# Kernel tuning notes

Measured on AMD Instinct MI355X. Metric: run time of the kernel, lower is better.

## Reference

```python
import jax, jax.numpy as jnp
import numpy as np

N, E, D, H, C, B, G = 50000, 800000, 128, 256, 40, 3, 2
EPS = 1e-5


def setup_inputs() -> dict:
    key = jax.random.key(0)
    ks = jax.random.split(key, 32)
    rn = lambda k, s: jax.random.normal(k, s, dtype=jnp.float32)
    inp = {
        'x': rn(ks[0], (N, D)),
        'edge_index': jax.random.randint(ks[1], (2, E), 0, N, dtype=jnp.int64),
        'Wp': rn(ks[2], (D, H)), 'bp': rn(ks[3], (H,)),
        'W1l': rn(ks[4], (B, H, H)), 'b1l': rn(ks[5], (B, H)), 'W1r': rn(ks[6], (B, H, H)),
        'W2l': rn(ks[7], (B, H, H)), 'b2l': rn(ks[8], (B, H)), 'W2r': rn(ks[9], (B, H, H)),
        'bn1_g': rn(ks[10], (B, H)), 'bn1_b': rn(ks[11], (B, H)), 'bn1_m': rn(ks[12], (B, H)),
        'bn1_v': jax.random.uniform(ks[13], (B, H), dtype=jnp.float32),
        'bn2_g': rn(ks[14], (B, H)), 'bn2_b': rn(ks[15], (B, H)), 'bn2_m': rn(ks[16], (B, H)),
        'bn2_v': jax.random.uniform(ks[17], (B, H), dtype=jnp.float32),
        'gate_W': rn(ks[18], (G, H, H)), 'gate_b': rn(ks[19], (G, H)),
        'Wc1': rn(ks[20], (H, H // 2)), 'bc1': rn(ks[21], (H // 2,)),
        'Wc2': rn(ks[22], (H // 2, C)), 'bc2': rn(ks[23], (C,)),
    }
    return inp


def _sage(x, src, dst, Wl, bl, Wr):
    # PyG SAGEConv (mean aggr): lin_l(mean_{j in N(i)} x_j) + lin_r(x_i)
    agg = jax.ops.segment_sum(x[src], dst, num_segments=N)  # [N,H]
    cnt = jax.ops.segment_sum(jnp.ones((src.shape[0],), x.dtype), dst, num_segments=N)
    mean = agg / jnp.maximum(cnt, 1.0)[:, None]
    return mean @ Wl + bl + x @ Wr


def _bn(x, g, b, m, v):
    return (x - m) * (g * jax.lax.rsqrt(v + EPS)) + b


def reference(x, edge_index, Wp, bp, W1l, b1l, W1r, W2l, b2l, W2r,
              bn1_g, bn1_b, bn1_m, bn1_v, bn2_g, bn2_b, bn2_m, bn2_v,
              gate_W, gate_b, Wc1, bc1, Wc2, bc2):
    src, dst = edge_index[0], edge_index[1]
    prev = x @ Wp + bp  # input projection [N,H]
    for i in range(B):
        res = prev
        h = jax.nn.relu(_bn(_sage(prev, src, dst, W1l[i], b1l[i], W1r[i]),
                            bn1_g[i], bn1_b[i], bn1_m[i], bn1_v[i]))
        h = jax.nn.relu(_bn(_sage(h, src, dst, W2l[i], b2l[i], W2r[i]),
                            bn2_g[i], bn2_b[i], bn2_m[i], bn2_v[i]))
        cur = h + res
        if i > 0:
            gate = jax.nn.sigmoid(prev @ gate_W[i - 1] + gate_b[i - 1])
            cur = gate * prev + (1.0 - gate) * cur
        prev = cur
    return jax.nn.relu(prev @ Wc1 + bc1) @ Wc2 + bc2  # [N,C]
```

## Files before the change

kernel.cpp:

```cpp
#include <hip/hip_runtime.h>
#include <hip/hip_bf16.h>
#include <cstdint>

#define NNODES 50000
#define MPAD   50048
#define NEDGES 800000
#define DIN 128
#define HID 256
#define NCLS 40
#define NBLK 3
#define EPSV 1e-5f

typedef __bf16 bf16x8 __attribute__((ext_vector_type(8)));
typedef float  f32x4  __attribute__((ext_vector_type(4)));
typedef unsigned short us4v __attribute__((ext_vector_type(4)));
typedef unsigned short us8v __attribute__((ext_vector_type(8)));

__device__ __forceinline__ unsigned short bf_rtn(float x) {
  unsigned u = __float_as_uint(x);
  return (unsigned short)((u + 0x7fffu + ((u >> 16) & 1u)) >> 16);
}
__device__ __forceinline__ float bf_f(unsigned short h) {
  return __uint_as_float((unsigned)h << 16);
}
__device__ __forceinline__ void split4(float4 a, us4v& h, us4v& m, us4v& l) {
  float v[4] = {a.x, a.y, a.z, a.w};
#pragma unroll
  for (int i = 0; i < 4; i++) {
    unsigned short hh = bf_rtn(v[i]);
    float r1 = v[i] - bf_f(hh);
    unsigned short mm = bf_rtn(r1);
    float r2 = r1 - bf_f(mm);
    h[i] = hh; m[i] = mm; l[i] = bf_rtn(r2);
  }
}

__device__ __forceinline__ void glds16(const void* gsrc, void* ldst) {
  __builtin_amdgcn_global_load_lds((const __attribute__((address_space(1))) void*)gsrc,
                                   (__attribute__((address_space(3))) void*)ldst,
                                   16, 0, 0);
}

__global__ void hist_kernel(const int* __restrict__ dst, int* __restrict__ cnt, int E) {
  int e = blockIdx.x * blockDim.x + threadIdx.x;
  if (e < E) atomicAdd(&cnt[dst[e]], 1);
}

__global__ void scan_kernel(const int* __restrict__ cnt, int* __restrict__ row_ptr,
                            float* __restrict__ inv_cnt, int N) {
  __shared__ int sums[1024];
  int t = threadIdx.x;
  int chunk = (N + 1023) >> 10;
  int beg = t * chunk;
  int end = beg + chunk; if (end > N) end = N;
  int s = 0;
  for (int i = beg; i < end; ++i) s += cnt[i];
  sums[t] = s;
  __syncthreads();
  for (int off = 1; off < 1024; off <<= 1) {
    int v = 0;
    if (t >= off) v = sums[t - off];
    __syncthreads();
    sums[t] += v;
    __syncthreads();
  }
  int run = (t == 0) ? 0 : sums[t - 1];
  for (int i = beg; i < end; ++i) {
    row_ptr[i] = run;
    int c = cnt[i];
    inv_cnt[i] = 1.0f / (float)(c > 0 ? c : 1);
    run += c;
  }
  if (t == 1023) row_ptr[N] = run;
}

__global__ void fill_kernel(const int* __restrict__ src, const int* __restrict__ dst,
                            const int* __restrict__ row_ptr, int* __restrict__ fillc,
                            int* __restrict__ col, int E) {
  int e = blockIdx.x * blockDim.x + threadIdx.x;
  if (e < E) {
    int d = dst[e];
    int pos = atomicAdd(&fillc[d], 1);
    col[row_ptr[d] + pos] = src[e];
  }
}

__global__ __launch_bounds__(256)
void agg_kernel(const float* __restrict__ x, float* __restrict__ out,
                const int* __restrict__ row_ptr, const int* __restrict__ col,
                const float* __restrict__ inv_cnt) {
  int n = blockIdx.x;
  int h = threadIdx.x;
  int beg = row_ptr[n], end = row_ptr[n + 1];
  float s = 0.0f;
  for (int j = beg; j < end; ++j) {
    int c = col[j];
    s += x[(long)c * HID + h];
  }
  out[(long)n * HID + h] = s * inv_cnt[n];
}

__global__ void fold_kernel(const float* __restrict__ b1l, const float* __restrict__ g1,
                            const float* __restrict__ bb1, const float* __restrict__ m1,
                            const float* __restrict__ v1,
                            const float* __restrict__ b2l, const float* __restrict__ g2,
                            const float* __restrict__ bb2, const float* __restrict__ m2,
                            const float* __restrict__ v2,
                            float* __restrict__ S1, float* __restrict__ T1,
                            float* __restrict__ S2, float* __restrict__ T2) {
  int idx = blockIdx.x * 256 + threadIdx.x;
  float s1 = g1[idx] * rsqrtf(v1[idx] + EPSV);
  S1[idx] = s1;
  T1[idx] = (b1l[idx] - m1[idx]) * s1 + bb1[idx];
  float s2 = g2[idx] * rsqrtf(v2[idx] + EPSV);
  S2[idx] = s2;
  T2[idx] = (b2l[idx] - m2[idx]) * s2 + bb2[idx];
}

#define PREP_TOTAL 368640
struct PrepDescs {
  const float* src[16];
  unsigned dst_off[16];
  int N[16];
  int cum[16];
};
__global__ __launch_bounds__(256)
void prep_kernel(PrepDescs pd, char* out) {
  int i = blockIdx.x * 256 + threadIdx.x;
  if (i >= PREP_TOTAL) return;
  int j = 0;
  while (i >= pd.cum[j]) j++;
  int li = i - (j ? pd.cum[j - 1] : 0);
  int c = li % 12;
  int t = li / 12;
  int N = pd.N[j];
  int n = t % N;
  int kt = t / N;
  const float* src = pd.src[j];
  char* base = out + pd.dst_off[j] + (size_t)kt * N * 192;
  int p, k8;
  size_t addr;
  if (c < 8) {
    int d = c ^ (n & 7);
    p = d >> 2; k8 = d & 3;
    addr = (size_t)n * 128 + (size_t)c * 16;
  } else {
    p = 2; k8 = c - 8;
    addr = (size_t)N * 128 + ((size_t)k8 * N + n) * 16;
  }
  us8v v;
#pragma unroll
  for (int xj = 0; xj < 8; xj++) {
    float w = src[(size_t)(kt * 32 + k8 * 8 + xj) * N + n];
    unsigned short h = bf_rtn(w);
    if (p == 0) { v[xj] = h; continue; }
    float r1 = w - bf_f(h);
    unsigned short m = bf_rtn(r1);
    v[xj] = (p == 1) ? m : bf_rtn(r1 - bf_f(m));
  }
  *reinterpret_cast<us8v*>(base + addr) = v;
}

template<int BM, int BN, bool GATED>
__global__ __launch_bounds__(512)
void gemm_mfma(const float* __restrict__ A1, const char* __restrict__ B1, int K1,
               const float* __restrict__ A2, const char* __restrict__ B2, int K2,
               const char* __restrict__ BG, const float* __restrict__ Gb,
               const float* __restrict__ Sc, const float* __restrict__ Tc,
               const float* __restrict__ resid, float* __restrict__ C,
               int Mguard, int do_relu) {
  constexpr int WN = BN / 64;
  constexpr int WM = 8 / WN;
  constexpr int RB = BM / WM;
  constexpr int MT = RB / 16;
  constexpr int APITCH = 104;
  constexpr int AL = (BM * 32) / 2048;
  constexpr int NG = (BN * 24) / 1024;
  __shared__ __align__(16) unsigned short A_lds[2][BM][APITCH];
  __shared__ __align__(16) char B_lds[2][BN * 192];
  const int tid  = threadIdx.x;
  const int wv   = tid >> 6;
  const int lane = tid & 63;
  const int l15  = lane & 15;
  const int quad = lane >> 4;
  const int wm   = wv / WN;
  const int wn   = wv % WN;
  const int m0   = blockIdx.x * BM;
  const int sr   = tid >> 3;
  const int skc  = (tid & 7) * 4;

  f32x4 acc1[MT][4];
#pragma unroll
  for (int i = 0; i < MT; i++)
#pragma unroll
    for (int j = 0; j < 4; j++) acc1[i][j] = (f32x4){0.f, 0.f, 0.f, 0.f};
  f32x4 acc2[GATED ? MT : 1][GATED ? 4 : 1];
  if constexpr (GATED) {
#pragma unroll
    for (int i = 0; i < MT; i++)
#pragma unroll
      for (int j = 0; j < 4; j++) acc2[i][j] = (f32x4){0.f, 0.f, 0.f, 0.f};
  }

  int buf = 0;

  auto issueB = [&](const char* Bp, int kt, int b) {
    const char* bsrc = Bp + (size_t)kt * (BN * 192) + wv * (BN * 24) + (size_t)lane * 16;
    char* bdst = &B_lds[b][wv * (BN * 24)];
#pragma unroll
    for (int j = 0; j < NG; ++j)
      glds16(bsrc + j * 1024, bdst + j * 1024);
  };
  auto storeA = [&](float4 (&a)[AL], int b) {
#pragma unroll
    for (int i = 0; i < AL; i++) {
      us4v h4, m4, l4;
      split4(a[i], h4, m4, l4);
      unsigned short* rp = &A_lds[b][sr + i * 64][0];
      *reinterpret_cast<us4v*>(rp + skc)      = h4;
      *reinterpret_cast<us4v*>(rp + 32 + skc) = m4;
      *reinterpret_cast<us4v*>(rp + 64 + skc) = l4;
    }
  };

  auto phase = [&](const float* __restrict__ A, const char* __restrict__ Bp,
                   int K, f32x4 (&acc)[MT][4]) {
    const int KT = K / 32;
    bool g[AL];
    const float* ap[AL];
#pragma unroll
    for (int i = 0; i < AL; i++) {
      int row = m0 + sr + i * 64;
      g[i] = row < Mguard;
      ap[i] = A + (size_t)row * K + skc;
    }
    issueB(Bp, 0, buf);
    {
      float4 a[AL];
#pragma unroll
      for (int i = 0; i < AL; i++)
        a[i] = g[i] ? *reinterpret_cast<const float4*>(ap[i]) : make_float4(0.f, 0.f, 0.f, 0.f);
      storeA(a, buf);
    }
    for (int kt = 0; kt < KT; ++kt) {
      __syncthreads();
      const bool pf = (kt + 1 < KT);
      float4 a[AL];
      if (pf) {
        issueB(Bp, kt + 1, buf ^ 1);
#pragma unroll
        for (int i = 0; i < AL; i++)
          a[i] = g[i] ? *reinterpret_cast<const float4*>(ap[i] + (kt + 1) * 32)
                      : make_float4(0.f, 0.f, 0.f, 0.f);
      }
      bf16x8 ah[MT], am[MT], al[MT];
#pragma unroll
      for (int mt = 0; mt < MT; mt++) {
        const unsigned short* rp = &A_lds[buf][wm * RB + mt * 16 + l15][0];
        ah[mt] = *reinterpret_cast<const bf16x8*>(rp + quad * 8);
        am[mt] = *reinterpret_cast<const bf16x8*>(rp + 32 + quad * 8);
        al[mt] = *reinterpret_cast<const bf16x8*>(rp + 64 + quad * 8);
      }
#pragma unroll
      for (int nt = 0; nt < 4; nt++) {
        int n = wn * 64 + nt * 16 + l15;
        int sw = n & 7;
        const char* rb = &B_lds[buf][(size_t)n * 128];
        bf16x8 bh = *reinterpret_cast<const bf16x8*>(rb + ((quad ^ sw) * 16));
        bf16x8 bm = *reinterpret_cast<const bf16x8*>(rb + (((4 + quad) ^ sw) * 16));
        bf16x8 bl = *reinterpret_cast<const bf16x8*>(
            &B_lds[buf][(size_t)BN * 128 + ((size_t)quad * BN + n) * 16]);
#pragma unroll
        for (int mt = 0; mt < MT; mt++) {
          acc[mt][nt] = __builtin_amdgcn_mfma_f32_16x16x32_bf16(ah[mt], bh, acc[mt][nt], 0, 0, 0);
          acc[mt][nt] = __builtin_amdgcn_mfma_f32_16x16x32_bf16(ah[mt], bm, acc[mt][nt], 0, 0, 0);
          acc[mt][nt] = __builtin_amdgcn_mfma_f32_16x16x32_bf16(am[mt], bh, acc[mt][nt], 0, 0, 0);
          acc[mt][nt] = __builtin_amdgcn_mfma_f32_16x16x32_bf16(am[mt], bm, acc[mt][nt], 0, 0, 0);
          acc[mt][nt] = __builtin_amdgcn_mfma_f32_16x16x32_bf16(ah[mt], bl, acc[mt][nt], 0, 0, 0);
          acc[mt][nt] = __builtin_amdgcn_mfma_f32_16x16x32_bf16(al[mt], bh, acc[mt][nt], 0, 0, 0);
        }
      }
      if (pf) storeA(a, buf ^ 1);
      buf ^= 1;
    }
  };

  phase(A1, B1, K1, acc1);
  if (A2) phase(A2, B2, K2, acc1);
  if constexpr (GATED) phase(resid, BG, HID, acc2);

#pragma unroll
  for (int nt = 0; nt < 4; nt++) {
    int colc = wn * 64 + nt * 16 + l15;
    float sc = Sc ? Sc[colc] : 1.0f;
    float tc = Tc[colc];
    float gb = 0.0f;
    if constexpr (GATED) gb = Gb[colc];
#pragma unroll
    for (int mt = 0; mt < MT; mt++) {
#pragma unroll
      for (int r = 0; r < 4; r++) {
        int row = m0 + wm * RB + mt * 16 + quad * 4 + r;
        size_t base = (size_t)row * BN + colc;
        float v = acc1[mt][nt][r] * sc + tc;
        if (do_relu) v = fmaxf(v, 0.0f);
        if constexpr (GATED) {
          float p = resid[base];
          float g = 1.0f / (1.0f + __expf(-(acc2[mt][nt][r] + gb)));
          v = g * p + (1.0f - g) * (v + p);
        } else if (resid) {
          v += resid[base];
        }
        C[base] = v;
      }
    }
  }
}

__global__ __launch_bounds__(256)
void classifier2(const float* __restrict__ Tin, const float* __restrict__ W,
                 const float* __restrict__ bias, float* __restrict__ out, int M) {
  __shared__ float Ws[DIN * NCLS];
  __shared__ float bs[NCLS];
  __shared__ float Ts[64][DIN + 4];
  int tid = threadIdx.x;
  for (int i = tid; i < DIN * NCLS; i += 256) Ws[i] = W[i];
  if (tid < NCLS) bs[tid] = bias[tid];
  int row0 = blockIdx.x * 64;
  for (int idx = tid; idx < 64 * (DIN / 4); idx += 256) {
    int r = idx / (DIN / 4);
    int c4 = idx % (DIN / 4);
    float4 v = make_float4(0.f, 0.f, 0.f, 0.f);
    if (row0 + r < M) v = *reinterpret_cast<const float4*>(Tin + (long)(row0 + r) * DIN + c4 * 4);
    *reinterpret_cast<float4*>(&Ts[r][c4 * 4]) = v;
  }
  __syncthreads();
  int r = tid >> 2;
  int c0 = (tid & 3) * 10;
  float s[10];
#pragma unroll
  for (int c = 0; c < 10; c++) s[c] = bs[c0 + c];
  for (int k = 0; k < DIN; k++) {
    float a = Ts[r][k];
#pragma unroll
    for (int c = 0; c < 10; c++) s[c] = fmaf(a, Ws[k * NCLS + c0 + c], s[c]);
  }
  if (row0 + r < M) {
#pragma unroll
    for (int c = 0; c < 10; c++) out[(long)(row0 + r) * NCLS + c0 + c] = s[c];
  }
}

extern "C" void kernel_launch(void* const* d_in, const int* in_sizes, int n_in,
                              void* d_out, int out_size, void* d_ws, size_t ws_size,
                              hipStream_t stream) {
  const float* x      = (const float*)d_in[0];
  const int*   ei     = (const int*)d_in[1];
  const float* Wp     = (const float*)d_in[2];
  const float* bp     = (const float*)d_in[3];
  const float* W1l    = (const float*)d_in[4];
  const float* b1l    = (const float*)d_in[5];
  const float* W1r    = (const float*)d_in[6];
  const float* W2l    = (const float*)d_in[7];
  const float* b2l    = (const float*)d_in[8];
  const float* W2r    = (const float*)d_in[9];
  const float* bn1_g  = (const float*)d_in[10];
  const float* bn1_b  = (const float*)d_in[11];
  const float* bn1_m  = (const float*)d_in[12];
  const float* bn1_v  = (const float*)d_in[13];
  const float* bn2_g  = (const float*)d_in[14];
  const float* bn2_b  = (const float*)d_in[15];
  const float* bn2_m  = (const float*)d_in[16];
  const float* bn2_v  = (const float*)d_in[17];
  const float* gate_W = (const float*)d_in[18];
  const float* gate_b = (const float*)d_in[19];
  const float* Wc1    = (const float*)d_in[20];
  const float* bc1    = (const float*)d_in[21];
  const float* Wc2    = (const float*)d_in[22];
  const float* bc2    = (const float*)d_in[23];
  const int* srcp = ei;
  const int* dstp = ei + NEDGES;

  char* wsb = (char*)d_ws;
  size_t off = 0;
  auto alloc = [&](size_t bytes) -> void* {
    void* p = wsb + off;
    off += (bytes + 255) & ~(size_t)255;
    return p;
  };
  float* X0 = (float*)alloc((size_t)MPAD * HID * 4);
  float* X1 = (float*)alloc((size_t)MPAD * HID * 4);
  float* X2 = (float*)alloc((size_t)MPAD * HID * 4);
  char* prep = (char*)alloc(5898240);
  int* cnt     = (int*)alloc((size_t)NNODES * 4 * 2);
  int* fillc   = cnt + NNODES;
  int* row_ptr = (int*)alloc((size_t)(NNODES + 1) * 4);
  float* inv   = (float*)alloc((size_t)NNODES * 4);
  int* col     = (int*)alloc((size_t)NEDGES * 4);
  float* S1 = (float*)alloc(NBLK * HID * 4);
  float* T1 = (float*)alloc(NBLK * HID * 4);
  float* S2 = (float*)alloc(NBLK * HID * 4);
  float* T2 = (float*)alloc(NBLK * HID * 4);

  auto poff = [](int idx) -> unsigned {
    if (idx == 0) return 0;
    return 196608u + (unsigned)(idx - 1) * 393216u;
  };
  const char* prepWp  = prep + poff(0);
  auto prepW1l = [&](int i) { return prep + poff(1 + i); };
  auto prepW1r = [&](int i) { return prep + poff(4 + i); };
  auto prepW2l = [&](int i) { return prep + poff(7 + i); };
  auto prepW2r = [&](int i) { return prep + poff(10 + i); };
  auto prepGate = [&](int g) { return prep + poff(13 + g); };
  const char* prepWc1 = prep + poff(15);

  PrepDescs pd;
  {
    int c = 0, k = 0;
    auto add = [&](const float* s, int N, int chunks, unsigned doff) {
      pd.src[k] = s; pd.N[k] = N; c += chunks; pd.cum[k] = c; pd.dst_off[k] = doff; k++;
    };
    add(Wp, 256, 12288, poff(0));
    for (int i = 0; i < 3; i++) add(W1l + (size_t)i * 65536, 256, 24576, poff(1 + i));
    for (int i = 0; i < 3; i++) add(W1r + (size_t)i * 65536, 256, 24576, poff(4 + i));
    for (int i = 0; i < 3; i++) add(W2l + (size_t)i * 65536, 256, 24576, poff(7 + i));
    for (int i = 0; i < 3; i++) add(W2r + (size_t)i * 65536, 256, 24576, poff(10 + i));
    for (int g = 0; g < 2; g++) add(gate_W + (size_t)g * 65536, 256, 24576, poff(13 + g));
    add(Wc1, 128, 12288, poff(15));
  }

  hipMemsetAsync(cnt, 0, (size_t)NNODES * 4 * 2, stream);
  int eb = (NEDGES + 255) / 256;
  hist_kernel<<<eb, 256, 0, stream>>>(dstp, cnt, NEDGES);
  scan_kernel<<<1, 1024, 0, stream>>>(cnt, row_ptr, inv, NNODES);
  fill_kernel<<<eb, 256, 0, stream>>>(srcp, dstp, row_ptr, fillc, col, NEDGES);
  fold_kernel<<<3, 256, 0, stream>>>(b1l, bn1_g, bn1_b, bn1_m, bn1_v,
                                     b2l, bn2_g, bn2_b, bn2_m, bn2_v, S1, T1, S2, T2);
  prep_kernel<<<PREP_TOTAL / 256, 256, 0, stream>>>(pd, prep);

  int gm128 = MPAD / 128;
  int gm64  = MPAD / 64;
  gemm_mfma<128, 256, false><<<gm128, 512, 0, stream>>>(
      x, prepWp, DIN, nullptr, nullptr, 0, nullptr, nullptr,
      nullptr, bp, nullptr, X0, NNODES, 0);

  float* bufs[3] = {X0, X1, X2};
  int prev = 0;
  for (int i = 0; i < NBLK; ++i) {
    int bm = (prev + 1) % 3;
    int bh = (prev + 2) % 3;
    float* P  = bufs[prev];
    float* Mb = bufs[bm];
    float* Hb = bufs[bh];
    agg_kernel<<<NNODES, 256, 0, stream>>>(P, Mb, row_ptr, col, inv);
    gemm_mfma<128, 256, false><<<gm128, 512, 0, stream>>>(
        Mb, prepW1l(i), HID, P, prepW1r(i), HID, nullptr, nullptr,
        S1 + i * HID, T1 + i * HID, nullptr, Hb, MPAD, 1);
    agg_kernel<<<NNODES, 256, 0, stream>>>(Hb, Mb, row_ptr, col, inv);
    if (i == 0) {
      gemm_mfma<128, 256, false><<<gm128, 512, 0, stream>>>(
          Mb, prepW2l(0), HID, Hb, prepW2r(0), HID, nullptr, nullptr,
          S2, T2, P, Mb, MPAD, 1);
    } else {
      gemm_mfma<64, 256, true><<<gm64, 512, 0, stream>>>(
          Mb, prepW2l(i), HID, Hb, prepW2r(i), HID,
          prepGate(i - 1), gate_b + (size_t)(i - 1) * HID,
          S2 + i * HID, T2 + i * HID, P, Mb, MPAD, 1);
    }
    prev = bm;
  }
  float* P  = bufs[prev];
  float* Tb = bufs[(prev + 1) % 3];
  gemm_mfma<128, 128, false><<<gm128, 512, 0, stream>>>(
      P, prepWc1, HID, nullptr, nullptr, 0, nullptr, nullptr,
      nullptr, bc1, nullptr, Tb, MPAD, 1);
  classifier2<<<gm128 * 2, 256, 0, stream>>>(Tb, Wc2, bc2, (float*)d_out, NNODES);
}
```

Before: 2.124 ms.

## Retile GEMM to 64x128 blocks with 256 threads and N-split grid

Replaces the templated BM/BN GEMM with a fixed 64-row by 128-column tile using 4 waves. The output columns are split across blocks, so the grid grows to roughly 1564 blocks for better CU occupancy, and the LDS footprint per block drops. B fragments are now loaded from LDS before the next-tile prefetch is issued, so the prefetch overlaps the MFMA work. A fourth activation buffer is added so the second-conv output no longer writes in place over its aggregation input. The cost is that the A tile is reloaded and re-split for each column half, which adds global traffic and conversion work.

```diff
diff --git a/kernel.cpp b/kernel.cpp
--- a/kernel.cpp
+++ b/kernel.cpp
@@ -161,43 +161,38 @@
   *reinterpret_cast<us8v*>(base + addr) = v;
 }
 
-template<int BM, int BN, bool GATED>
-__global__ __launch_bounds__(512)
+template<bool GATED>
+__global__ __launch_bounds__(256)
 void gemm_mfma(const float* __restrict__ A1, const char* __restrict__ B1, int K1,
                const float* __restrict__ A2, const char* __restrict__ B2, int K2,
                const char* __restrict__ BG, const float* __restrict__ Gb,
                const float* __restrict__ Sc, const float* __restrict__ Tc,
                const float* __restrict__ resid, float* __restrict__ C,
-               int Mguard, int do_relu) {
-  constexpr int WN = BN / 64;
-  constexpr int WM = 8 / WN;
-  constexpr int RB = BM / WM;
-  constexpr int MT = RB / 16;
-  constexpr int APITCH = 104;
-  constexpr int AL = (BM * 32) / 2048;
-  constexpr int NG = (BN * 24) / 1024;
-  __shared__ __align__(16) unsigned short A_lds[2][BM][APITCH];
-  __shared__ __align__(16) char B_lds[2][BN * 192];
+               int Bn, int Mguard, int do_relu) {
+  __shared__ __align__(16) unsigned short A_lds[2][64][104];
+  __shared__ __align__(16) char B_lds[2][24576];
   const int tid  = threadIdx.x;
   const int wv   = tid >> 6;
   const int lane = tid & 63;
   const int l15  = lane & 15;
   const int quad = lane >> 4;
-  const int wm   = wv / WN;
-  const int wn   = wv % WN;
-  const int m0   = blockIdx.x * BM;
+  const int NC   = Bn >> 7;
+  const int n0   = (blockIdx.x % NC) * 128;
+  const int m0   = (blockIdx.x / NC) * 64;
+  const int wm   = wv >> 1;
+  const int wn   = wv & 1;
   const int sr   = tid >> 3;
   const int skc  = (tid & 7) * 4;
 
-  f32x4 acc1[MT][4];
-#pragma unroll
-  for (int i = 0; i < MT; i++)
+  f32x4 acc1[2][4];
+#pragma unroll
+  for (int i = 0; i < 2; i++)
 #pragma unroll
     for (int j = 0; j < 4; j++) acc1[i][j] = (f32x4){0.f, 0.f, 0.f, 0.f};
-  f32x4 acc2[GATED ? MT : 1][GATED ? 4 : 1];
+  f32x4 acc2[GATED ? 2 : 1][GATED ? 4 : 1];
   if constexpr (GATED) {
 #pragma unroll
-    for (int i = 0; i < MT; i++)
+    for (int i = 0; i < 2; i++)
 #pragma unroll
       for (int j = 0; j < 4; j++) acc2[i][j] = (f32x4){0.f, 0.f, 0.f, 0.f};
   }
@@ -205,18 +200,28 @@
   int buf = 0;
 
   auto issueB = [&](const char* Bp, int kt, int b) {
-    const char* bsrc = Bp + (size_t)kt * (BN * 192) + wv * (BN * 24) + (size_t)lane * 16;
-    char* bdst = &B_lds[b][wv * (BN * 24)];
-#pragma unroll
-    for (int j = 0; j < NG; ++j)
-      glds16(bsrc + j * 1024, bdst + j * 1024);
+    const char* tb = Bp + (size_t)kt * ((size_t)Bn * 192);
+#pragma unroll
+    for (int j = 0; j < 6; ++j) {
+      int o = wv * 6144 + j * 1024;
+      const char* src;
+      if (o < 16384) {
+        src = tb + (size_t)n0 * 128 + o;
+      } else {
+        int ol = o - 16384;
+        int k8 = ol >> 11;
+        int within = ol & 2047;
+        src = tb + (size_t)Bn * 128 + (size_t)k8 * Bn * 16 + (size_t)n0 * 16 + within;
+      }
+      glds16(src + (size_t)lane * 16, &B_lds[b][o]);
+    }
   };
-  auto storeA = [&](float4 (&a)[AL], int b) {
-#pragma unroll
-    for (int i = 0; i < AL; i++) {
+  auto storeA = [&](float4 (&a)[2], int b) {
+#pragma unroll
+    for (int i = 0; i < 2; i++) {
       us4v h4, m4, l4;
       split4(a[i], h4, m4, l4);
-      unsigned short* rp = &A_lds[b][sr + i * 64][0];
+      unsigned short* rp = &A_lds[b][sr + i * 32][0];
       *reinterpret_cast<us4v*>(rp + skc)      = h4;
       *reinterpret_cast<us4v*>(rp + 32 + skc) = m4;
       *reinterpret_cast<us4v*>(rp + 64 + skc) = l4;
@@ -224,60 +229,64 @@
   };
 
   auto phase = [&](const float* __restrict__ A, const char* __restrict__ Bp,
-                   int K, f32x4 (&acc)[MT][4]) {
+                   int K, f32x4 (&acc)[2][4]) {
     const int KT = K / 32;
-    bool g[AL];
-    const float* ap[AL];
-#pragma unroll
-    for (int i = 0; i < AL; i++) {
-      int row = m0 + sr + i * 64;
+    bool g[2];
+    const float* ap[2];
+#pragma unroll
+    for (int i = 0; i < 2; i++) {
+      int row = m0 + sr + i * 32;
       g[i] = row < Mguard;
       ap[i] = A + (size_t)row * K + skc;
     }
     issueB(Bp, 0, buf);
     {
-      float4 a[AL];
-#pragma unroll
-      for (int i = 0; i < AL; i++)
+      float4 a[2];
+#pragma unroll
+      for (int i = 0; i < 2; i++)
         a[i] = g[i] ? *reinterpret_cast<const float4*>(ap[i]) : make_float4(0.f, 0.f, 0.f, 0.f);
       storeA(a, buf);
     }
     for (int kt = 0; kt < KT; ++kt) {
       __syncthreads();
-      const bool pf = (kt + 1 < KT);
-      float4 a[AL];
-      if (pf) {
-        issueB(Bp, kt + 1, buf ^ 1);
-#pragma unroll
-        for (int i = 0; i < AL; i++)
-          a[i] = g[i] ? *reinterpret_cast<const float4*>(ap[i] + (kt + 1) * 32)
-                      : make_float4(0.f, 0.f, 0.f, 0.f);
-      }
-      bf16x8 ah[MT], am[MT], al[MT];
-#pragma unroll
-      for (int mt = 0; mt < MT; mt++) {
-        const unsigned short* rp = &A_lds[buf][wm * RB + mt * 16 + l15][0];
+      bf16x8 ah[2], am[2], al[2];
+#pragma unroll
+      for (int mt = 0; mt < 2; mt++) {
+        const unsigned short* rp = &A_lds[buf][wm * 32 + mt * 16 + l15][0];
         ah[mt] = *reinterpret_cast<const bf16x8*>(rp + quad * 8);
         am[mt] = *reinterpret_cast<const bf16x8*>(rp + 32 + quad * 8);
         al[mt] = *reinterpret_cast<const bf16x8*>(rp + 64 + quad * 8);
       }
+      bf16x8 bh[4], bm_[4], bl[4];
 #pragma unroll
       for (int nt = 0; nt < 4; nt++) {
-        int n = wn * 64 + nt * 16 + l15;
-        int sw = n & 7;
-        const char* rb = &B_lds[buf][(size_t)n * 128];
-        bf16x8 bh = *reinterpret_cast<const bf16x8*>(rb + ((quad ^ sw) * 16));
-        bf16x8 bm = *reinterpret_cast<const bf16x8*>(rb + (((4 + quad) ^ sw) * 16));
-        bf16x8 bl = *reinterpret_cast<const bf16x8*>(
-            &B_lds[buf][(size_t)BN * 128 + ((size_t)quad * BN + n) * 16]);
-#pragma unroll
-        for (int mt = 0; mt < MT; mt++) {
-          acc[mt][nt] = __builtin_amdgcn_mfma_f32_16x16x32_bf16(ah[mt], bh, acc[mt][nt], 0, 0, 0);
-          acc[mt][nt] = __builtin_amdgcn_mfma_f32_16x16x32_bf16(ah[mt], bm, acc[mt][nt], 0, 0, 0);
-          acc[mt][nt] = __builtin_amdgcn_mfma_f32_16x16x32_bf16(am[mt], bh, acc[mt][nt], 0, 0, 0);
-          acc[mt][nt] = __builtin_amdgcn_mfma_f32_16x16x32_bf16(am[mt], bm, acc[mt][nt], 0, 0, 0);
-          acc[mt][nt] = __builtin_amdgcn_mfma_f32_16x16x32_bf16(ah[mt], bl, acc[mt][nt], 0, 0, 0);
-          acc[mt][nt] = __builtin_amdgcn_mfma_f32_16x16x32_bf16(al[mt], bh, acc[mt][nt], 0, 0, 0);
+        int ln = wn * 64 + nt * 16 + l15;
+        int sw = ln & 7;
+        const char* rb = &B_lds[buf][(size_t)ln * 128];
+        bh[nt]  = *reinterpret_cast<const bf16x8*>(rb + ((quad ^ sw) * 16));
+        bm_[nt] = *reinterpret_cast<const bf16x8*>(rb + (((4 + quad) ^ sw) * 16));
+        bl[nt]  = *reinterpret_cast<const bf16x8*>(
+            &B_lds[buf][16384 + ((size_t)quad * 128 + ln) * 16]);
+      }
+      const bool pf = (kt + 1 < KT);
+      float4 a[2];
+      if (pf) {
+        issueB(Bp, kt + 1, buf ^ 1);
+#pragma unroll
+        for (int i = 0; i < 2; i++)
+          a[i] = g[i] ? *reinterpret_cast<const float4*>(ap[i] + (kt + 1) * 32)
+                      : make_float4(0.f, 0.f, 0.f, 0.f);
+      }
+#pragma unroll
+      for (int nt = 0; nt < 4; nt++) {
+#pragma unroll
+        for (int mt = 0; mt < 2; mt++) {
+          acc[mt][nt] = __builtin_amdgcn_mfma_f32_16x16x32_bf16(ah[mt], bh[nt],  acc[mt][nt], 0, 0, 0);
+          acc[mt][nt] = __builtin_amdgcn_mfma_f32_16x16x32_bf16(ah[mt], bm_[nt], acc[mt][nt], 0, 0, 0);
+          acc[mt][nt] = __builtin_amdgcn_mfma_f32_16x16x32_bf16(am[mt], bh[nt],  acc[mt][nt], 0, 0, 0);
+          acc[mt][nt] = __builtin_amdgcn_mfma_f32_16x16x32_bf16(am[mt], bm_[nt], acc[mt][nt], 0, 0, 0);
+          acc[mt][nt] = __builtin_amdgcn_mfma_f32_16x16x32_bf16(ah[mt], bl[nt],  acc[mt][nt], 0, 0, 0);
+          acc[mt][nt] = __builtin_amdgcn_mfma_f32_16x16x32_bf16(al[mt], bh[nt],  acc[mt][nt], 0, 0, 0);
         }
       }
       if (pf) storeA(a, buf ^ 1);
@@ -291,17 +300,17 @@
 
 #pragma unroll
   for (int nt = 0; nt < 4; nt++) {
-    int colc = wn * 64 + nt * 16 + l15;
+    int colc = n0 + wn * 64 + nt * 16 + l15;
     float sc = Sc ? Sc[colc] : 1.0f;
     float tc = Tc[colc];
     float gb = 0.0f;
     if constexpr (GATED) gb = Gb[colc];
 #pragma unroll
-    for (int mt = 0; mt < MT; mt++) {
+    for (int mt = 0; mt < 2; mt++) {
 #pragma unroll
       for (int r = 0; r < 4; r++) {
-        int row = m0 + wm * RB + mt * 16 + quad * 4 + r;
-        size_t base = (size_t)row * BN + colc;
+        int row = m0 + wm * 32 + mt * 16 + quad * 4 + r;
+        size_t base = (size_t)row * Bn + colc;
         float v = acc1[mt][nt][r] * sc + tc;
         if (do_relu) v = fmaxf(v, 0.0f);
         if constexpr (GATED) {
@@ -391,6 +400,7 @@
   float* X0 = (float*)alloc((size_t)MPAD * HID * 4);
   float* X1 = (float*)alloc((size_t)MPAD * HID * 4);
   float* X2 = (float*)alloc((size_t)MPAD * HID * 4);
+  float* X3 = (float*)alloc((size_t)MPAD * HID * 4);
   char* prep = (char*)alloc(5898240);
   int* cnt     = (int*)alloc((size_t)NNODES * 4 * 2);
   int* fillc   = cnt + NNODES;
@@ -438,41 +448,43 @@
                                      b2l, bn2_g, bn2_b, bn2_m, bn2_v, S1, T1, S2, T2);
   prep_kernel<<<PREP_TOTAL / 256, 256, 0, stream>>>(pd, prep);
 
-  int gm128 = MPAD / 128;
-  int gm64  = MPAD / 64;
-  gemm_mfma<128, 256, false><<<gm128, 512, 0, stream>>>(
+  const int gmw = MPAD / 64;
+  const int g256 = gmw * 2;
+  gemm_mfma<false><<<g256, 256, 0, stream>>>(
       x, prepWp, DIN, nullptr, nullptr, 0, nullptr, nullptr,
-      nullptr, bp, nullptr, X0, NNODES, 0);
-
-  float* bufs[3] = {X0, X1, X2};
-  int prev = 0;
+      nullptr, bp, nullptr, X0, 256, NNODES, 0);
+
+  float* bufs[4] = {X0, X1, X2, X3};
+  int ip = 0;
   for (int i = 0; i < NBLK; ++i) {
-    int bm = (prev + 1) % 3;
-    int bh = (prev + 2) % 3;
-    float* P  = bufs[prev];
-    float* Mb = bufs[bm];
-    float* Hb = bufs[bh];
+    int im = (ip + 1) & 3;
+    int ih = (ip + 2) & 3;
+    int id = (ip + 3) & 3;
+    float* P  = bufs[ip];
+    float* Mb = bufs[im];
+    float* Hb = bufs[ih];
+    float* Db = bufs[id];
     agg_kernel<<<NNODES, 256, 0, stream>>>(P, Mb, row_ptr, col, inv);
-    gemm_mfma<128, 256, false><<<gm128, 512, 0, stream>>>(
+    gemm_mfma<false><<<g256, 256, 0, stream>>>(
         Mb, prepW1l(i), HID, P, prepW1r(i), HID, nullptr, nullptr,
-        S1 + i * HID, T1 + i * HID, nullptr, Hb, MPAD, 1);
+        S1 + i * HID, T1 + i * HID, nullptr, Hb, 256, MPAD, 1);
     agg_kernel<<<NNODES, 256, 0, stream>>>(Hb, Mb, row_ptr, col, inv);
     if (i == 0) {
-      gemm_mfma<128, 256, false><<<gm128, 512, 0, stream>>>(
+      gemm_mfma<false><<<g256, 256, 0, stream>>>(
           Mb, prepW2l(0), HID, Hb, prepW2r(0), HID, nullptr, nullptr,
-          S2, T2, P, Mb, MPAD, 1);
+          S2, T2, P, Db, 256, MPAD, 1);
     } else {
-      gemm_mfma<64, 256, true><<<gm64, 512, 0, stream>>>(
+      gemm_mfma<true><<<g256, 256, 0, stream>>>(
           Mb, prepW2l(i), HID, Hb, prepW2r(i), HID,
           prepGate(i - 1), gate_b + (size_t)(i - 1) * HID,
-          S2 + i * HID, T2 + i * HID, P, Mb, MPAD, 1);
-    }
-    prev = bm;
-  }
-  float* P  = bufs[prev];
-  float* Tb = bufs[(prev + 1) % 3];
-  gemm_mfma<128, 128, false><<<gm128, 512, 0, stream>>>(
+          S2 + i * HID, T2 + i * HID, P, Db, 256, MPAD, 1);
+    }
+    ip = id;
+  }
+  float* P  = bufs[ip];
+  float* Tb = bufs[(ip + 1) & 3];
+  gemm_mfma<false><<<gmw, 256, 0, stream>>>(
       P, prepWc1, HID, nullptr, nullptr, 0, nullptr, nullptr,
-      nullptr, bc1, nullptr, Tb, MPAD, 1);
-  classifier2<<<gm128 * 2, 256, 0, stream>>>(Tb, Wc2, bc2, (float*)d_out, NNODES);
-}
+      nullptr, bc1, nullptr, Tb, 128, MPAD, 1);
+  classifier2<<<gmw, 256, 0, stream>>>(Tb, Wc2, bc2, (float*)d_out, NNODES);
+}
```

New measurement: 2.107 ms. No clear change (-0.8%).
